# Kernel tuning notes

Measured on AMD Instinct MI355X. Metric: run time of the kernel, lower is better.

The kernel has to match this reference:

```python
import jax, jax.numpy as jnp
import numpy as np

EMBD = 1024
N_HEADS = 16
DK = EMBD // N_HEADS


def setup_inputs() -> dict:
    key = jax.random.key(0)
    ks = jax.random.split(key, 5)
    B, T = 2, 2048
    scale = 1.0 / np.sqrt(EMBD)
    x = jax.random.normal(ks[0], (B, T, EMBD), dtype=jnp.float32)
    W_qkv = jax.random.normal(ks[1], (EMBD, 3 * EMBD), dtype=jnp.float32) * scale
    b_qkv = jnp.zeros((3 * EMBD,), dtype=jnp.float32)
    W_proj = jax.random.normal(ks[2], (EMBD, EMBD), dtype=jnp.float32) * scale
    b_proj = jnp.zeros((EMBD,), dtype=jnp.float32)
    return {"x": x, "W_qkv": W_qkv, "b_qkv": b_qkv, "W_proj": W_proj, "b_proj": b_proj}


def reference(x, W_qkv, b_qkv, W_proj, b_proj):
    B, T, C = x.shape
    qkv = x @ W_qkv + b_qkv                      # [B, T, 3C]
    q, k, v = jnp.split(qkv, 3, axis=-1)
    # [B, H, T, dk]
    q = q.reshape(B, T, N_HEADS, DK).transpose(0, 2, 1, 3)
    k = k.reshape(B, T, N_HEADS, DK).transpose(0, 2, 1, 3)
    v = v.reshape(B, T, N_HEADS, DK).transpose(0, 2, 1, 3)
    att = jnp.einsum('bhqd,bhkd->bhqk', q, k) / np.sqrt(DK).astype(np.float32)
    causal = jnp.triu(jnp.full((T, T), -jnp.inf, dtype=att.dtype), k=1)
    att = jax.nn.softmax(att + causal, axis=-1)  # dropout p=0.0 -> identity
    y = jnp.einsum('bhqk,bhkd->bhqd', att, v)    # [B, H, T, dk]
    y = y.transpose(0, 2, 1, 3).reshape(B, T, C)
    y = y @ W_proj + b_proj
    return (y, (k, v))
```

## Files before the change

### kernel.cpp

```cpp
#include <hip/hip_runtime.h>
#include <hip/hip_bf16.h>

#define B_   2
#define T_   2048
#define C_   1024
#define H_   16
#define DK_  64

typedef __bf16 bf16x8 __attribute__((ext_vector_type(8)));
typedef float  f32x4  __attribute__((ext_vector_type(4)));
typedef unsigned short u16;
typedef u16 u16x4 __attribute__((ext_vector_type(4)));
typedef u16 u16x8 __attribute__((ext_vector_type(8)));

static __device__ __forceinline__ u16 f2bf(float f) {
    unsigned u = __float_as_uint(f);
    u += 0x7fffu + ((u >> 16) & 1u);
    return (u16)(u >> 16);
}
static __device__ __forceinline__ float bf2f(u16 h) {
    return __uint_as_float(((unsigned)h) << 16);
}

static __device__ __forceinline__ void async16(void* l, const void* g) {
    __builtin_amdgcn_global_load_lds(
        (const __attribute__((address_space(1))) unsigned int*)g,
        (__attribute__((address_space(3))) unsigned int*)l, 16, 0, 0);
}

__global__ __launch_bounds__(256) void pack_a_hl(const float* __restrict__ src, char* __restrict__ dst) {
    const int mt = blockIdx.x, kt = blockIdx.y, t = threadIdx.x;
    const int r = t >> 1, half = t & 1;
    const float* s = src + (size_t)(mt * 128 + r) * 1024 + kt * 32 + half * 16;
    float f[16];
    #pragma unroll
    for (int i = 0; i < 4; ++i) *(float4*)&f[i * 4] = ((const float4*)s)[i];
    u16 hi[16] __attribute__((aligned(16))), lo[16] __attribute__((aligned(16)));
    #pragma unroll
    for (int e = 0; e < 16; ++e) { hi[e] = f2bf(f[e]); lo[e] = f2bf(f[e] - bf2f(hi[e])); }
    char* tb = dst + ((size_t)mt * 32 + kt) * 16384;
    const int sw = (r & 7) << 4;
    #pragma unroll
    for (int j = 0; j < 2; ++j) {
        int g = half * 2 + j;
        *(u16x8*)(tb + ((r * 128 + g * 16) ^ sw))      = *(u16x8*)&hi[j * 8];
        *(u16x8*)(tb + ((r * 128 + 64 + g * 16) ^ sw)) = *(u16x8*)&lo[j * 8];
    }
}

__global__ __launch_bounds__(256) void pack_a_s(const float* __restrict__ src, char* __restrict__ dst) {
    const int mt = blockIdx.x, kt = blockIdx.y, t = threadIdx.x;
    const int r = t >> 1, half = t & 1;
    const float* s = src + (size_t)(mt * 128 + r) * 1024 + kt * 64 + half * 32;
    float f[32];
    #pragma unroll
    for (int i = 0; i < 8; ++i) *(float4*)&f[i * 4] = ((const float4*)s)[i];
    u16 hv[32] __attribute__((aligned(16)));
    #pragma unroll
    for (int e = 0; e < 32; ++e) hv[e] = f2bf(f[e]);
    char* tb = dst + ((size_t)mt * 16 + kt) * 16384;
    const int sw = (r & 7) << 4;
    #pragma unroll
    for (int j = 0; j < 4; ++j) {
        int g = half * 4 + j;
        *(u16x8*)(tb + ((r * 128 + g * 16) ^ sw)) = *(u16x8*)&hv[j * 8];
    }
}

template <int BKT>
__global__ __launch_bounds__(256) void pack_bt_hl(const float* __restrict__ W, char* __restrict__ dst,
                                                  int N, int nkt) {
    __shared__ float Ls[BKT][132];
    const int nt = blockIdx.x, kt = blockIdx.y, t = threadIdx.x;
    #pragma unroll
    for (int p = 0; p < BKT / 32; ++p) {
        int kr = p * 32 + (t >> 3), c8 = t & 7;
        const float* s = W + (size_t)(kt * BKT + kr) * N + nt * 128 + c8 * 16;
        #pragma unroll
        for (int i = 0; i < 4; ++i) *(float4*)&Ls[kr][c8 * 16 + i * 4] = ((const float4*)s)[i];
    }
    __syncthreads();
    const int nr = t >> 1, half = t & 1;
    constexpr int KH = BKT / 2;
    constexpr int ROWB = BKT * 4;
    constexpr int TILEB = 128 * ROWB;
    char* tb = dst + ((size_t)nt * nkt + kt) * TILEB;
    u16 hi[KH] __attribute__((aligned(16))), lo[KH] __attribute__((aligned(16)));
    #pragma unroll
    for (int e = 0; e < KH; ++e) {
        float x = Ls[half * KH + e][nr];
        hi[e] = f2bf(x); lo[e] = f2bf(x - bf2f(hi[e]));
    }
    const int sw = (nr & 7) << 4;
    #pragma unroll
    for (int j = 0; j < KH / 8; ++j) {
        int g = half * (KH / 8) + j;
        *(u16x8*)(tb + ((nr * ROWB + g * 16) ^ sw))            = *(u16x8*)&hi[j * 8];
        *(u16x8*)(tb + ((nr * ROWB + ROWB / 2 + g * 16) ^ sw)) = *(u16x8*)&lo[j * 8];
    }
}

__global__ __launch_bounds__(256, 2) void qkv_gemm_bf16(
    const char* __restrict__ xp, const char* __restrict__ wqp,
    const float* __restrict__ bqkv,
    float* __restrict__ qy, float* __restrict__ k_out, float* __restrict__ v_out)
{
    __shared__ __align__(16) char Alds[16384];
    __shared__ __align__(16) char Blds[16384];
    const int mt = blockIdx.x, nt = blockIdx.y;
    const int t = threadIdx.x, lane = t & 63, w = t >> 6;
    const int g = lane >> 4, r15 = lane & 15;
    const int wm = w >> 1, wn = w & 1;

    int aoff[4][2], boff[4][2];
    #pragma unroll
    for (int s = 0; s < 4; ++s) {
        int ar = wm * 64 + s * 16 + r15, sa = (ar & 7) << 4;
        aoff[s][0] = (ar * 128 + g * 16) ^ sa;
        aoff[s][1] = (ar * 128 + 64 + g * 16) ^ sa;
        int br = wn * 64 + s * 16 + r15, sb = (br & 7) << 4;
        boff[s][0] = (br * 128 + g * 16) ^ sb;
        boff[s][1] = (br * 128 + 64 + g * 16) ^ sb;
    }

    f32x4 acc[4][4];
    #pragma unroll
    for (int i = 0; i < 4; ++i)
        #pragma unroll
        for (int j = 0; j < 4; ++j) acc[i][j] = (f32x4){0.f, 0.f, 0.f, 0.f};

    const char* Abase = xp + (size_t)mt * 32 * 16384 + w * 4096 + lane * 16;
    const char* Bbase = wqp + (size_t)nt * 32 * 16384 + w * 4096 + lane * 16;
    char* la = Alds + w * 4096;
    char* lb = Blds + w * 4096;

    for (int kt = 0; kt < 32; ++kt) {
        #pragma unroll
        for (int i = 0; i < 4; ++i) {
            async16(la + i * 1024, Abase + kt * 16384 + i * 1024);
            async16(lb + i * 1024, Bbase + kt * 16384 + i * 1024);
        }
        __syncthreads();
        bf16x8 af[4][2], bf[4][2];
        #pragma unroll
        for (int s = 0; s < 4; ++s) {
            af[s][0] = *(const bf16x8*)(Alds + aoff[s][0]);
            af[s][1] = *(const bf16x8*)(Alds + aoff[s][1]);
            bf[s][0] = *(const bf16x8*)(Blds + boff[s][0]);
            bf[s][1] = *(const bf16x8*)(Blds + boff[s][1]);
        }
        #pragma unroll
        for (int i = 0; i < 4; ++i)
            #pragma unroll
            for (int j = 0; j < 4; ++j) {
                acc[i][j] = __builtin_amdgcn_mfma_f32_16x16x32_bf16(af[i][0], bf[j][0], acc[i][j], 0, 0, 0);
                acc[i][j] = __builtin_amdgcn_mfma_f32_16x16x32_bf16(af[i][0], bf[j][1], acc[i][j], 0, 0, 0);
                acc[i][j] = __builtin_amdgcn_mfma_f32_16x16x32_bf16(af[i][1], bf[j][0], acc[i][j], 0, 0, 0);
            }
        __syncthreads();
    }

    const int n0 = nt * 128;
    const int sec = n0 >> 10;
    float* kv = (sec == 1) ? k_out : v_out;
    #pragma unroll
    for (int i = 0; i < 4; ++i) {
        int mbase = mt * 128 + wm * 64 + i * 16 + g * 4;
        #pragma unroll
        for (int j = 0; j < 4; ++j) {
            int n = n0 + wn * 64 + j * 16 + r15;
            float bias = bqkv[n];
            int c = n & 1023;
            #pragma unroll
            for (int r = 0; r < 4; ++r) {
                int m = mbase + r;
                int bb = m >> 11, tt = m & 2047;
                float val = acc[i][j][r] + bias;
                if (sec == 0)
                    qy[((size_t)bb * T_ + tt) * C_ + c] = val;
                else
                    kv[(((size_t)bb * H_ + (c >> 6)) * T_ + tt) * DK_ + (c & 63)] = val;
            }
        }
    }
}

__global__ __launch_bounds__(256, 2) void proj_gemm_bf16(
    const char* __restrict__ yap, const char* __restrict__ wpp,
    const float* __restrict__ bp, float* __restrict__ y)
{
    __shared__ __align__(16) char Alds[16384];
    __shared__ __align__(16) char Blds[32768];
    const int mt = blockIdx.x, nt = blockIdx.y;
    const int t = threadIdx.x, lane = t & 63, w = t >> 6;
    const int g = lane >> 4, r15 = lane & 15;
    const int wm = w >> 1, wn = w & 1;

    int aoff[4][2], boffh[4][2], boffl[4][2];
    #pragma unroll
    for (int s = 0; s < 4; ++s) {
        int ar = wm * 64 + s * 16 + r15, sa = (ar & 7) << 4;
        int br = wn * 64 + s * 16 + r15, sb = (br & 7) << 4;
        #pragma unroll
        for (int kk = 0; kk < 2; ++kk) {
            aoff[s][kk]  = (ar * 128 + (kk * 4 + g) * 16) ^ sa;
            boffh[s][kk] = (br * 256 + (kk * 4 + g) * 16) ^ sb;
            boffl[s][kk] = (br * 256 + 128 + (kk * 4 + g) * 16) ^ sb;
        }
    }

    f32x4 acc[4][4];
    #pragma unroll
    for (int i = 0; i < 4; ++i)
        #pragma unroll
        for (int j = 0; j < 4; ++j) acc[i][j] = (f32x4){0.f, 0.f, 0.f, 0.f};

    const char* Abase = yap + (size_t)mt * 16 * 16384 + w * 4096 + lane * 16;
    const char* Bbase = wpp + (size_t)nt * 16 * 32768 + w * 8192 + lane * 16;
    char* la = Alds + w * 4096;
    char* lb = Blds + w * 8192;

    for (int kt = 0; kt < 16; ++kt) {
        #pragma unroll
        for (int i = 0; i < 4; ++i)
            async16(la + i * 1024, Abase + kt * 16384 + i * 1024);
        #pragma unroll
        for (int i = 0; i < 8; ++i)
            async16(lb + i * 1024, Bbase + kt * 32768 + i * 1024);
        __syncthreads();
        #pragma unroll
        for (int kk = 0; kk < 2; ++kk) {
            bf16x8 af[4], bh[4], bl[4];
            #pragma unroll
            for (int s = 0; s < 4; ++s) {
                af[s] = *(const bf16x8*)(Alds + aoff[s][kk]);
                bh[s] = *(const bf16x8*)(Blds + boffh[s][kk]);
                bl[s] = *(const bf16x8*)(Blds + boffl[s][kk]);
            }
            #pragma unroll
            for (int i = 0; i < 4; ++i)
                #pragma unroll
                for (int j = 0; j < 4; ++j) {
                    acc[i][j] = __builtin_amdgcn_mfma_f32_16x16x32_bf16(af[i], bh[j], acc[i][j], 0, 0, 0);
                    acc[i][j] = __builtin_amdgcn_mfma_f32_16x16x32_bf16(af[i], bl[j], acc[i][j], 0, 0, 0);
                }
        }
        __syncthreads();
    }

    #pragma unroll
    for (int i = 0; i < 4; ++i) {
        int mbase = mt * 128 + wm * 64 + i * 16 + g * 4;
        #pragma unroll
        for (int j = 0; j < 4; ++j) {
            int n = nt * 128 + wn * 64 + j * 16 + r15;
            float bias = bp[n];
            #pragma unroll
            for (int r = 0; r < 4; ++r)
                y[(size_t)(mbase + r) * 1024 + n] = acc[i][j][r] + bias;
        }
    }
}

#define QS_H 0
#define QS_L 8192
#define KS_H 16384
#define KS_L 24576
#define VT_H 32768
#define VT_L 40960
#define PS_H 49152
#define PS_L 57344

__global__ __launch_bounds__(256) void attn_mfma_kernel(
    const float* __restrict__ qy,
    const float* __restrict__ k_in,
    const float* __restrict__ v_in,
    float* __restrict__ yatt)
{
    __shared__ __align__(16) char lds[65536];

    const int bh   = blockIdx.x;
    const int qt   = 31 - (int)blockIdx.y;
    const int qb   = qt * 64;
    const int t    = threadIdx.x;
    const int lane = t & 63;
    const int w    = t >> 6;
    const int g    = lane >> 4;
    const int r15  = lane & 15;
    const int b    = bh >> 4, h = bh & 15;

    const float* Qb = qy + ((size_t)b * T_ + qb) * C_ + h * 64;
    const float* Kb = k_in + (size_t)bh * T_ * DK_;
    const float* Vb = v_in + (size_t)bh * T_ * DK_;

    #pragma unroll
    for (int di = 0; di < 4; ++di) {
        int fidx = di * 256 + t;
        int row  = fidx >> 4;
        int c4   = fidx & 15;
        float4 f = ((const float4*)(Qb + (size_t)row * C_))[c4];
        f.x *= 0.125f; f.y *= 0.125f; f.z *= 0.125f; f.w *= 0.125f;
        u16 h0 = f2bf(f.x), h1 = f2bf(f.y), h2 = f2bf(f.z), h3 = f2bf(f.w);
        u16 l0 = f2bf(f.x - bf2f(h0)), l1 = f2bf(f.y - bf2f(h1));
        u16 l2 = f2bf(f.z - bf2f(h2)), l3 = f2bf(f.w - bf2f(h3));
        int off = (row * 128 + c4 * 8) ^ ((row & 7) << 4);
        u16x4 hv = {h0, h1, h2, h3};
        u16x4 lv = {l0, l1, l2, l3};
        *(u16x4*)(lds + QS_H + off) = hv;
        *(u16x4*)(lds + QS_L + off) = lv;
    }
    __syncthreads();

    bf16x8 qfh[2], qfl[2];
    const int prow = w * 16 + r15;
    #pragma unroll
    for (int dc = 0; dc < 2; ++dc) {
        int off = (prow * 128 + dc * 64 + g * 16) ^ ((prow & 7) << 4);
        qfh[dc] = *(const bf16x8*)(lds + QS_H + off);
        qfl[dc] = *(const bf16x8*)(lds + QS_L + off);
    }

    f32x4 zero4 = {0.f, 0.f, 0.f, 0.f};
    f32x4 o[4];
    o[0] = zero4; o[1] = zero4; o[2] = zero4; o[3] = zero4;
    float mrun = -1e30f, lrun = 0.f;
    const int qglob = qb + w * 16 + r15;

    const int nt = qt + 1;
    for (int kt = 0; kt < nt; ++kt) {
        const int j0 = kt * 64;
        __syncthreads();
        #pragma unroll
        for (int di = 0; di < 4; ++di) {
            int fidx = di * 256 + t;
            int row  = fidx >> 4;
            int c4   = fidx & 15;
            float4 fk = ((const float4*)(Kb + (size_t)(j0 + row) * 64))[c4];
            u16 h0 = f2bf(fk.x), h1 = f2bf(fk.y), h2 = f2bf(fk.z), h3 = f2bf(fk.w);
            u16 l0 = f2bf(fk.x - bf2f(h0)), l1 = f2bf(fk.y - bf2f(h1));
            u16 l2 = f2bf(fk.z - bf2f(h2)), l3 = f2bf(fk.w - bf2f(h3));
            int off = (row * 128 + c4 * 8) ^ ((row & 7) << 4);
            u16x4 hv = {h0, h1, h2, h3};
            u16x4 lv = {l0, l1, l2, l3};
            *(u16x4*)(lds + KS_H + off) = hv;
            *(u16x4*)(lds + KS_L + off) = lv;

            float4 fv = ((const float4*)(Vb + (size_t)(j0 + row) * 64))[c4];
            float vv[4] = {fv.x, fv.y, fv.z, fv.w};
            #pragma unroll
            for (int j = 0; j < 4; ++j) {
                int jj = (j + t) & 3;
                float x = vv[jj];
                int dd  = c4 * 4 + jj;
                u16 hh = f2bf(x);
                u16 ll = f2bf(x - bf2f(hh));
                int offv = (dd * 128 + row * 2) ^ ((dd & 7) << 4);
                *(u16*)(lds + VT_H + offv) = hh;
                *(u16*)(lds + VT_L + offv) = ll;
            }
        }
        __syncthreads();

        float sv[4][4];
        const bool diag = (kt == qt);
        #pragma unroll
        for (int st = 0; st < 4; ++st) {
            f32x4 acc = zero4;
            int krow = st * 16 + r15;
            #pragma unroll
            for (int dc = 0; dc < 2; ++dc) {
                int off = (krow * 128 + dc * 64 + g * 16) ^ ((krow & 7) << 4);
                bf16x8 kh = *(const bf16x8*)(lds + KS_H + off);
                bf16x8 kl = *(const bf16x8*)(lds + KS_L + off);
                acc = __builtin_amdgcn_mfma_f32_16x16x32_bf16(kh, qfh[dc], acc, 0, 0, 0);
                acc = __builtin_amdgcn_mfma_f32_16x16x32_bf16(kh, qfl[dc], acc, 0, 0, 0);
                acc = __builtin_amdgcn_mfma_f32_16x16x32_bf16(kl, qfh[dc], acc, 0, 0, 0);
            }
            #pragma unroll
            for (int r = 0; r < 4; ++r) {
                float x = acc[r];
                if (diag) {
                    int kg = j0 + st * 16 + g * 4 + r;
                    if (kg > qglob) x = -1e30f;
                }
                sv[st][r] = x;
            }
        }

        float tm = sv[0][0];
        #pragma unroll
        for (int st = 0; st < 4; ++st)
            #pragma unroll
            for (int r = 0; r < 4; ++r) tm = fmaxf(tm, sv[st][r]);
        tm = fmaxf(tm, __shfl_xor(tm, 16));
        tm = fmaxf(tm, __shfl_xor(tm, 32));
        float mnew = fmaxf(mrun, tm);
        float resc = __expf(mrun - mnew);
        mrun = mnew;
        lrun *= resc;
        o[0] *= resc; o[1] *= resc; o[2] *= resc; o[3] *= resc;

        float ps = 0.f;
        #pragma unroll
        for (int st = 0; st < 4; ++st)
            #pragma unroll
            for (int r = 0; r < 4; ++r) {
                float p = __expf(sv[st][r] - mnew);
                sv[st][r] = p;
                ps += p;
            }
        ps += __shfl_xor(ps, 16);
        ps += __shfl_xor(ps, 32);
        lrun += ps;

        #pragma unroll
        for (int st = 0; st < 4; ++st) {
            u16 h0 = f2bf(sv[st][0]), h1 = f2bf(sv[st][1]);
            u16 h2 = f2bf(sv[st][2]), h3 = f2bf(sv[st][3]);
            u16 l0 = f2bf(sv[st][0] - bf2f(h0)), l1 = f2bf(sv[st][1] - bf2f(h1));
            u16 l2 = f2bf(sv[st][2] - bf2f(h2)), l3 = f2bf(sv[st][3] - bf2f(h3));
            int off = (prow * 128 + (st * 16 + g * 4) * 2) ^ ((prow & 7) << 4);
            u16x4 hv = {h0, h1, h2, h3};
            u16x4 lv = {l0, l1, l2, l3};
            *(u16x4*)(lds + PS_H + off) = hv;
            *(u16x4*)(lds + PS_L + off) = lv;
        }

        bf16x8 pfh[2], pfl[2];
        #pragma unroll
        for (int kc = 0; kc < 2; ++kc) {
            int off = (prow * 128 + kc * 64 + g * 16) ^ ((prow & 7) << 4);
            pfh[kc] = *(const bf16x8*)(lds + PS_H + off);
            pfl[kc] = *(const bf16x8*)(lds + PS_L + off);
        }
        #pragma unroll
        for (int dt = 0; dt < 4; ++dt) {
            int vrow = dt * 16 + r15;
            #pragma unroll
            for (int kc = 0; kc < 2; ++kc) {
                int off = (vrow * 128 + kc * 64 + g * 16) ^ ((vrow & 7) << 4);
                bf16x8 vh = *(const bf16x8*)(lds + VT_H + off);
                bf16x8 vl = *(const bf16x8*)(lds + VT_L + off);
                o[dt] = __builtin_amdgcn_mfma_f32_16x16x32_bf16(vh, pfh[kc], o[dt], 0, 0, 0);
                o[dt] = __builtin_amdgcn_mfma_f32_16x16x32_bf16(vh, pfl[kc], o[dt], 0, 0, 0);
                o[dt] = __builtin_amdgcn_mfma_f32_16x16x32_bf16(vl, pfh[kc], o[dt], 0, 0, 0);
            }
        }
    }

    const float inv = 1.f / lrun;
    float* yo = yatt + ((size_t)b * T_ + qglob) * C_ + h * DK_;
    #pragma unroll
    for (int dt = 0; dt < 4; ++dt)
        #pragma unroll
        for (int r = 0; r < 4; ++r)
            yo[dt * 16 + g * 4 + r] = o[dt][r] * inv;
}

extern "C" void kernel_launch(void* const* d_in, const int* in_sizes, int n_in,
                              void* d_out, int out_size, void* d_ws, size_t ws_size,
                              hipStream_t stream) {
    const float* x     = (const float*)d_in[0];
    const float* Wqkv  = (const float*)d_in[1];
    const float* bqkv  = (const float*)d_in[2];
    const float* Wproj = (const float*)d_in[3];
    const float* bproj = (const float*)d_in[4];

    float* y     = (float*)d_out;
    float* qy    = y;
    float* k_out = y + (size_t)4194304;
    float* v_out = y + (size_t)8388608;

    char*  ws   = (char*)d_ws;
    char*  xp   = ws;
    float* yatt = (float*)ws;
    char*  wqp  = ws + ((size_t)16 << 20);
    char*  yap  = ws + ((size_t)16 << 20);
    char*  wpp  = ws + ((size_t)28 << 20);

    pack_a_hl   <<<dim3(32, 32), 256, 0, stream>>>(x, xp);
    pack_bt_hl<32><<<dim3(24, 32), 256, 0, stream>>>(Wqkv, wqp, 3072, 32);
    pack_bt_hl<64><<<dim3(8, 16), 256, 0, stream>>>(Wproj, wpp, 1024, 16);
    qkv_gemm_bf16<<<dim3(32, 24), 256, 0, stream>>>(xp, wqp, bqkv, qy, k_out, v_out);
    attn_mfma_kernel<<<dim3(32, 32), 256, 0, stream>>>(qy, k_out, v_out, yatt);
    pack_a_s    <<<dim3(32, 16), 256, 0, stream>>>(yatt, yap);
    proj_gemm_bf16<<<dim3(32, 8), 256, 0, stream>>>(yap, wpp, bproj, y);
}
```

Before: 341.2 us.

## Pre-pack K/V into bf16 hi/lo swizzled tiles and async-load them in attention

Measured after the change: 292.0 us. 14.4% less time.

```diff
diff --git a/kernel.cpp b/kernel.cpp
--- a/kernel.cpp
+++ b/kernel.cpp
@@ -97,6 +97,53 @@
         int g = half * (KH / 8) + j;
         *(u16x8*)(tb + ((nr * ROWB + g * 16) ^ sw))            = *(u16x8*)&hi[j * 8];
         *(u16x8*)(tb + ((nr * ROWB + ROWB / 2 + g * 16) ^ sw)) = *(u16x8*)&lo[j * 8];
+    }
+}
+
+__global__ __launch_bounds__(256) void kv_pack(
+    const float* __restrict__ k_in, const float* __restrict__ v_in,
+    char* __restrict__ kp, char* __restrict__ vp)
+{
+    __shared__ float Ls[64][68];
+    const int bh = blockIdx.x, kt = blockIdx.y, t = threadIdx.x;
+    const float* Kb = k_in + (size_t)bh * T_ * DK_ + (size_t)kt * 64 * DK_;
+    const float* Vb = v_in + (size_t)bh * T_ * DK_ + (size_t)kt * 64 * DK_;
+    char* ktb = kp + ((size_t)bh * 32 + kt) * 16384;
+    char* vtb = vp + ((size_t)bh * 32 + kt) * 16384;
+    const int row = t >> 2, qtr = t & 3;
+
+    {
+        float f[16];
+        #pragma unroll
+        for (int i = 0; i < 4; ++i)
+            *(float4*)&f[i * 4] = ((const float4*)(Kb + (size_t)row * 64 + qtr * 16))[i];
+        u16 hi[16] __attribute__((aligned(16))), lo[16] __attribute__((aligned(16)));
+        #pragma unroll
+        for (int e = 0; e < 16; ++e) { hi[e] = f2bf(f[e]); lo[e] = f2bf(f[e] - bf2f(hi[e])); }
+        const int sw = (row & 7) << 4;
+        *(u16x8*)(ktb + ((row * 128 + qtr * 32) ^ sw))             = *(u16x8*)&hi[0];
+        *(u16x8*)(ktb + ((row * 128 + qtr * 32 + 16) ^ sw))        = *(u16x8*)&hi[8];
+        *(u16x8*)(ktb + 8192 + ((row * 128 + qtr * 32) ^ sw))      = *(u16x8*)&lo[0];
+        *(u16x8*)(ktb + 8192 + ((row * 128 + qtr * 32 + 16) ^ sw)) = *(u16x8*)&lo[8];
+    }
+
+    #pragma unroll
+    for (int i = 0; i < 4; ++i)
+        *(float4*)&Ls[row][qtr * 16 + i * 4] = ((const float4*)(Vb + (size_t)row * 64 + qtr * 16))[i];
+    __syncthreads();
+    {
+        const int dd = t >> 2, tc2 = t & 3;
+        float f[16];
+        #pragma unroll
+        for (int k = 0; k < 16; ++k) f[k] = Ls[tc2 * 16 + k][dd];
+        u16 hi[16] __attribute__((aligned(16))), lo[16] __attribute__((aligned(16)));
+        #pragma unroll
+        for (int e = 0; e < 16; ++e) { hi[e] = f2bf(f[e]); lo[e] = f2bf(f[e] - bf2f(hi[e])); }
+        const int sw = (dd & 7) << 4;
+        *(u16x8*)(vtb + ((dd * 128 + tc2 * 32) ^ sw))             = *(u16x8*)&hi[0];
+        *(u16x8*)(vtb + ((dd * 128 + tc2 * 32 + 16) ^ sw))        = *(u16x8*)&hi[8];
+        *(u16x8*)(vtb + 8192 + ((dd * 128 + tc2 * 32) ^ sw))      = *(u16x8*)&lo[0];
+        *(u16x8*)(vtb + 8192 + ((dd * 128 + tc2 * 32 + 16) ^ sw)) = *(u16x8*)&lo[8];
     }
 }
 
@@ -262,22 +309,19 @@
     }
 }
 
-#define QS_H 0
-#define QS_L 8192
+#define PS_H 0
+#define PS_L 8192
 #define KS_H 16384
 #define KS_L 24576
 #define VT_H 32768
 #define VT_L 40960
-#define PS_H 49152
-#define PS_L 57344
 
 __global__ __launch_bounds__(256) void attn_mfma_kernel(
-    const float* __restrict__ qy,
-    const float* __restrict__ k_in,
-    const float* __restrict__ v_in,
-    float* __restrict__ yatt)
+    float* qyatt,
+    const char* __restrict__ Kp,
+    const char* __restrict__ Vp)
 {
-    __shared__ __align__(16) char lds[65536];
+    __shared__ __align__(16) char lds[49152];
 
     const int bh   = blockIdx.x;
     const int qt   = 31 - (int)blockIdx.y;
@@ -289,9 +333,7 @@
     const int r15  = lane & 15;
     const int b    = bh >> 4, h = bh & 15;
 
-    const float* Qb = qy + ((size_t)b * T_ + qb) * C_ + h * 64;
-    const float* Kb = k_in + (size_t)bh * T_ * DK_;
-    const float* Vb = v_in + (size_t)bh * T_ * DK_;
+    const float* Qb = qyatt + ((size_t)b * T_ + qb) * C_ + h * 64;
 
     #pragma unroll
     for (int di = 0; di < 4; ++di) {
@@ -306,8 +348,8 @@
         int off = (row * 128 + c4 * 8) ^ ((row & 7) << 4);
         u16x4 hv = {h0, h1, h2, h3};
         u16x4 lv = {l0, l1, l2, l3};
-        *(u16x4*)(lds + QS_H + off) = hv;
-        *(u16x4*)(lds + QS_L + off) = lv;
+        *(u16x4*)(lds + PS_H + off) = hv;
+        *(u16x4*)(lds + PS_L + off) = lv;
     }
     __syncthreads();
 
@@ -316,8 +358,8 @@
     #pragma unroll
     for (int dc = 0; dc < 2; ++dc) {
         int off = (prow * 128 + dc * 64 + g * 16) ^ ((prow & 7) << 4);
-        qfh[dc] = *(const bf16x8*)(lds + QS_H + off);
-        qfl[dc] = *(const bf16x8*)(lds + QS_L + off);
+        qfh[dc] = *(const bf16x8*)(lds + PS_H + off);
+        qfl[dc] = *(const bf16x8*)(lds + PS_L + off);
     }
 
     f32x4 zero4 = {0.f, 0.f, 0.f, 0.f};
@@ -330,33 +372,15 @@
     for (int kt = 0; kt < nt; ++kt) {
         const int j0 = kt * 64;
         __syncthreads();
-        #pragma unroll
-        for (int di = 0; di < 4; ++di) {
-            int fidx = di * 256 + t;
-            int row  = fidx >> 4;
-            int c4   = fidx & 15;
-            float4 fk = ((const float4*)(Kb + (size_t)(j0 + row) * 64))[c4];
-            u16 h0 = f2bf(fk.x), h1 = f2bf(fk.y), h2 = f2bf(fk.z), h3 = f2bf(fk.w);
-            u16 l0 = f2bf(fk.x - bf2f(h0)), l1 = f2bf(fk.y - bf2f(h1));
-            u16 l2 = f2bf(fk.z - bf2f(h2)), l3 = f2bf(fk.w - bf2f(h3));
-            int off = (row * 128 + c4 * 8) ^ ((row & 7) << 4);
-            u16x4 hv = {h0, h1, h2, h3};
-            u16x4 lv = {l0, l1, l2, l3};
-            *(u16x4*)(lds + KS_H + off) = hv;
-            *(u16x4*)(lds + KS_L + off) = lv;
-
-            float4 fv = ((const float4*)(Vb + (size_t)(j0 + row) * 64))[c4];
-            float vv[4] = {fv.x, fv.y, fv.z, fv.w};
-            #pragma unroll
-            for (int j = 0; j < 4; ++j) {
-                int jj = (j + t) & 3;
-                float x = vv[jj];
-                int dd  = c4 * 4 + jj;
-                u16 hh = f2bf(x);
-                u16 ll = f2bf(x - bf2f(hh));
-                int offv = (dd * 128 + row * 2) ^ ((dd & 7) << 4);
-                *(u16*)(lds + VT_H + offv) = hh;
-                *(u16*)(lds + VT_L + offv) = ll;
+        {
+            const char* Kg = Kp + ((size_t)bh * 32 + kt) * 16384 + w * 4096 + lane * 16;
+            const char* Vg = Vp + ((size_t)bh * 32 + kt) * 16384 + w * 4096 + lane * 16;
+            char* lk = lds + KS_H + w * 4096;
+            char* lv = lds + VT_H + w * 4096;
+            #pragma unroll
+            for (int i = 0; i < 4; ++i) {
+                async16(lk + i * 1024, Kg + i * 1024);
+                async16(lv + i * 1024, Vg + i * 1024);
             }
         }
         __syncthreads();
@@ -449,7 +473,7 @@
     }
 
     const float inv = 1.f / lrun;
-    float* yo = yatt + ((size_t)b * T_ + qglob) * C_ + h * DK_;
+    float* yo = qyatt + ((size_t)b * T_ + qglob) * C_ + h * DK_;
     #pragma unroll
     for (int dt = 0; dt < 4; ++dt)
         #pragma unroll
@@ -467,22 +491,23 @@
     const float* bproj = (const float*)d_in[4];
 
     float* y     = (float*)d_out;
-    float* qy    = y;
     float* k_out = y + (size_t)4194304;
     float* v_out = y + (size_t)8388608;
 
-    char*  ws   = (char*)d_ws;
-    char*  xp   = ws;
-    float* yatt = (float*)ws;
-    char*  wqp  = ws + ((size_t)16 << 20);
-    char*  yap  = ws + ((size_t)16 << 20);
-    char*  wpp  = ws + ((size_t)28 << 20);
-
-    pack_a_hl   <<<dim3(32, 32), 256, 0, stream>>>(x, xp);
+    char* ws = (char*)d_ws;
+    char* xp  = ws;
+    char* wqp = ws + ((size_t)16 << 20);
+    char* Kp  = ws;
+    char* Vp  = ws + ((size_t)16 << 20);
+    char* yap = ws;
+    char* wpp = ws + ((size_t)8 << 20);
+
+    pack_a_hl     <<<dim3(32, 32), 256, 0, stream>>>(x, xp);
     pack_bt_hl<32><<<dim3(24, 32), 256, 0, stream>>>(Wqkv, wqp, 3072, 32);
+    qkv_gemm_bf16 <<<dim3(32, 24), 256, 0, stream>>>(xp, wqp, bqkv, y, k_out, v_out);
+    kv_pack       <<<dim3(32, 32), 256, 0, stream>>>(k_out, v_out, Kp, Vp);
+    attn_mfma_kernel<<<dim3(32, 32), 256, 0, stream>>>(y, Kp, Vp);
+    pack_a_s      <<<dim3(32, 16), 256, 0, stream>>>(y, yap);
     pack_bt_hl<64><<<dim3(8, 16), 256, 0, stream>>>(Wproj, wpp, 1024, 16);
-    qkv_gemm_bf16<<<dim3(32, 24), 256, 0, stream>>>(xp, wqp, bqkv, qy, k_out, v_out);
-    attn_mfma_kernel<<<dim3(32, 32), 256, 0, stream>>>(qy, k_out, v_out, yatt);
-    pack_a_s    <<<dim3(32, 16), 256, 0, stream>>>(yatt, yap);
     proj_gemm_bf16<<<dim3(32, 8), 256, 0, stream>>>(yap, wpp, bproj, y);
 }
```
